# Kernel optimization log

Measured on AMD Instinct MI355X. Metric: run time of the kernel, lower is better.

## Reference

```python
import jax, jax.numpy as jnp
import numpy as np

B, N, DIM = 4, 16384, 3
HID = 128            # hidden_dim
CDIM = 128           # feature_dim
RESO = 128           # plane_resolution
R2 = RESO * RESO
NBLK = 5             # n_blocks


def setup_inputs() -> dict:
    key = jax.random.key(0)
    ks = jax.random.split(key, 8)
    s = 0.02
    return {
        "points": jax.random.uniform(ks[0], (B, N, DIM), jnp.float32),  # normalized to [0,1)
        "fc_pos_w": jax.random.normal(ks[1], (2 * HID, DIM), jnp.float32) * s,
        "fc_pos_b": jnp.zeros((2 * HID,), jnp.float32),
        "blk_fc0_w": jax.random.normal(ks[2], (NBLK, HID, 2 * HID), jnp.float32) * s,
        "blk_fc0_b": jnp.zeros((NBLK, HID), jnp.float32),
        "blk_fc1_w": jax.random.normal(ks[3], (NBLK, HID, HID), jnp.float32) * s,
        "blk_fc1_b": jnp.zeros((NBLK, HID), jnp.float32),
        "blk_sc_w": jax.random.normal(ks[4], (NBLK, HID, 2 * HID), jnp.float32) * s,
        "fc_c_w": jax.random.normal(ks[5], (CDIM, HID), jnp.float32) * s,
        "fc_c_b": jnp.zeros((CDIM,), jnp.float32),
    }


def _coord2index(coord_xy):
    # coordinate2index: (coord * reso).long(), then x + reso * y
    g = jnp.clip((coord_xy * RESO).astype(jnp.int32), 0, RESO - 1)  # (B, N, 2)
    return g[..., 0] + RESO * g[..., 1]  # (B, N)


def _resblock(x, w0, b0, w1, b1, ws):
    # ResnetBlockFC: shortcut(x) + fc_1(relu(fc_0(relu(x))))
    h = jax.nn.relu(x) @ w0.T + b0          # (B, N, HID)
    dx = jax.nn.relu(h) @ w1.T + b1         # (B, N, HID)
    return x @ ws.T + dx


def _forward(points, fc_pos_w, fc_pos_b, blk_fc0_w, blk_fc0_b,
             blk_fc1_w, blk_fc1_b, blk_sc_w, fc_c_w, fc_c_b):
    idx = _coord2index(points[..., :2])          # (B, N) int32 plane-bin ids
    net = points @ fc_pos_w.T + fc_pos_b          # (B, N, 2*HID)
    net = _resblock(net, blk_fc0_w[0], blk_fc0_b[0], blk_fc1_w[0], blk_fc1_b[0], blk_sc_w[0])

    seg_max = jax.vmap(lambda f, i: jax.ops.segment_max(f, i, num_segments=R2))
    for k in range(1, NBLK):
        bins = seg_max(net, idx)                                  # (B, R2, HID); empty bins -inf, never gathered
        pooled = jnp.take_along_axis(bins, idx[:, :, None], axis=1)  # (B, N, HID)
        net = _resblock(jnp.concatenate([net, pooled], axis=2),
                        blk_fc0_w[k], blk_fc0_b[k], blk_fc1_w[k], blk_fc1_b[k], blk_sc_w[k])

    net = jax.nn.relu(net) @ fc_c_w.T + fc_c_b    # (B, N, CDIM)

    # generate_plane_features: scatter_mean into zero-initialized plane
    seg_sum = jax.vmap(lambda f, i: jax.ops.segment_sum(f, i, num_segments=R2))
    sums = seg_sum(net, idx)                                      # (B, R2, CDIM)
    cnt = seg_sum(jnp.ones(idx.shape + (1,), net.dtype), idx)     # (B, R2, 1)
    mean = sums / jnp.maximum(cnt, 1.0)                           # empty bins stay 0
    return jnp.transpose(mean, (0, 2, 1)).reshape(B, CDIM, RESO, RESO)


def reference(points, fc_pos_w, fc_pos_b, blk_fc0_w, blk_fc0_b,
              blk_fc1_w, blk_fc1_b, blk_sc_w, fc_c_w, fc_c_b):
    return _forward(points, fc_pos_w, fc_pos_b, blk_fc0_w, blk_fc0_b,
                    blk_fc1_w, blk_fc1_b, blk_sc_w, fc_c_w, fc_c_b)
```

## Files before the change

### kernel.cpp

```cpp
#include <hip/hip_runtime.h>

#define NBATCH 4
#define NPTS   16384
#define BN     (NBATCH * NPTS)

typedef __attribute__((ext_vector_type(8))) _Float16 half8;
typedef __attribute__((ext_vector_type(4))) float f32x4;

#define INV4096 2.44140625e-4f

__device__ __forceinline__ void splith(float x, _Float16& h, _Float16& l) {
  float ax = __builtin_fabsf(x);
  if (ax < 6.1035e-5f) {
    unsigned short sb = (unsigned short)((__float_as_uint(x) >> 16) & 0x8000u);
    h = __builtin_bit_cast(_Float16, sb);
    l = (_Float16)(x * 4096.f);
  } else {
    _Float16 hh = (_Float16)x;
    h = hh;
    l = (_Float16)((x - (float)hh) * 4096.f);
  }
}
__device__ __forceinline__ void splith8(const float v[8], half8& hi, half8& lo) {
  #pragma unroll
  for (int j = 0; j < 8; ++j) { _Float16 h, l; splith(v[j], h, l); hi[j] = h; lo[j] = l; }
}

__device__ __forceinline__ half8 relu8(half8 sgn, half8 v) {
  uint4 s = __builtin_bit_cast(uint4, sgn);
  uint4 x = __builtin_bit_cast(uint4, v);
  unsigned* sp = (unsigned*)&s;
  unsigned* xp = (unsigned*)&x;
  uint4 out;
  unsigned* op = (unsigned*)&out;
  #pragma unroll
  for (int w = 0; w < 4; ++w) {
    unsigned m = sp[w] & 0x80008000u;
    unsigned drop = (m - (m >> 15)) | m;
    op[w] = xp[w] & ~drop;
  }
  return __builtin_bit_cast(half8, out);
}

__global__ void k_zero4(float4* __restrict__ p, int n4) {
  int g = blockIdx.x * 256 + threadIdx.x;
  if (g < n4) p[g] = make_float4(0.f, 0.f, 0.f, 0.f);
}

__device__ __forceinline__ int bin_of(const float* __restrict__ pts, int g) {
  float px = pts[g * 3 + 0], py = pts[g * 3 + 1];
  int xi = (int)(px * 128.f); xi = xi < 0 ? 0 : (xi > 127 ? 127 : xi);
  int yi = (int)(py * 128.f); yi = yi < 0 ? 0 : (yi > 127 ? 127 : yi);
  return xi + (yi << 7);
}

__global__ void k_idx(const float* __restrict__ pts, int* __restrict__ cnti) {
  int g = blockIdx.x * 256 + threadIdx.x;
  if (g >= BN) return;
  int b = g >> 14;
  atomicAdd(&cnti[(b << 14) + bin_of(pts, g)], 1);
}

__global__ void k_scan(const int* __restrict__ cnti, int* __restrict__ off,
                       int* __restrict__ cursor) {
  __shared__ int part[256];
  const int b = blockIdx.x, t = threadIdx.x;
  const int base = b << 14;
  int s = 0;
  #pragma unroll 8
  for (int i = 0; i < 64; ++i) s += cnti[base + t * 64 + i];
  part[t] = s;
  __syncthreads();
  for (int o = 1; o < 256; o <<= 1) {
    int v = (t >= o) ? part[t - o] : 0;
    __syncthreads();
    part[t] += v;
    __syncthreads();
  }
  int run = base + (t == 0 ? 0 : part[t - 1]);
  #pragma unroll 8
  for (int i = 0; i < 64; ++i) {
    int g = base + t * 64 + i;
    off[g] = run;
    cursor[g] = run;
    run += cnti[g];
  }
}

__global__ void k_scatter(const float* __restrict__ pts, int* __restrict__ cursor,
                          int* __restrict__ perm, int* __restrict__ sbin) {
  int p = blockIdx.x * 256 + threadIdx.x;
  if (p >= BN) return;
  int b = p >> 14;
  int id = bin_of(pts, p);
  int pos = atomicAdd(&cursor[(b << 14) + id], 1);
  perm[pos] = p;
  sbin[pos] = id;
}

__device__ __forceinline__ void pack_slot(const float* __restrict__ src, int K,
                                          _Float16* __restrict__ dhi, int NK,
                                          int slot) {
  int fpt = (K >> 5) << 6;
  int t = slot / fpt, rem = slot - t * fpt;
  int s = rem >> 6, lane = rem & 63;
  int row = (t << 4) + (lane & 15);
  int k0 = (s << 5) + ((lane >> 4) << 3);
  float v[8];
  #pragma unroll
  for (int j = 0; j < 8; ++j) v[j] = src[row * K + k0 + j];
  half8 hi, lo; splith8(v, hi, lo);
  *(half8*)&dhi[(size_t)slot << 3] = hi;
  *(half8*)&dhi[((size_t)slot << 3) + NK] = lo;
}

__global__ void k_pack(const float* __restrict__ fc0w, const float* __restrict__ scw,
                       const float* __restrict__ fc1w, const float* __restrict__ fccw,
                       _Float16* __restrict__ wp) {
  int g = blockIdx.x * 256 + threadIdx.x;
  if (g < 20480) {
    int l = g >> 12, slot = g & 4095;
    pack_slot(fc0w + (size_t)l * 32768, 256, wp + (size_t)l * 65536, 32768, slot);
  } else if (g < 40960) {
    int g2 = g - 20480; int l = g2 >> 12, slot = g2 & 4095;
    pack_slot(scw + (size_t)l * 32768, 256, wp + 327680 + (size_t)l * 65536, 32768, slot);
  } else if (g < 51200) {
    int g2 = g - 40960; int l = g2 >> 11, slot = g2 & 2047;
    pack_slot(fc1w + (size_t)l * 16384, 128, wp + 655360 + (size_t)l * 32768, 16384, slot);
  } else {
    int slot = g - 51200;
    pack_slot(fccw, 128, wp + 819200, 16384, slot);
  }
}

template <int SRC, int MODE>
__launch_bounds__(256, 4)
__global__ void k_rb(const float* __restrict__ pts, const float* __restrict__ netIn,
                     const int* __restrict__ perm, const int* __restrict__ sbin,
                     const int* __restrict__ off_, const int* __restrict__ cnti_,
                     const float* __restrict__ posw, const float* __restrict__ posb,
                     const _Float16* __restrict__ w0p, const float* __restrict__ b0,
                     const _Float16* __restrict__ w1p, const float* __restrict__ b1,
                     const _Float16* __restrict__ wsp,
                     float* __restrict__ netOut,
                     const _Float16* __restrict__ fccp, const float* __restrict__ fccb,
                     float* __restrict__ sums) {
  extern __shared__ _Float16 smem[];
  _Float16* Ahi = smem;
  _Float16* Alo = smem + 8192;
  const int tid = threadIdx.x;
  const int lane = tid & 63, wave = tid >> 6;
  const int p0 = blockIdx.x << 5;
  const int b = p0 >> 14;

  #pragma unroll
  for (int i = 0; i < 4; ++i) {
    int sidx = tid + (i << 8);
    int m = sidx >> 5, kslot = sidx & 31, k0 = kslot << 3;
    float v[8];
    if (SRC == 0) {
      const float* pp = &pts[(size_t)perm[p0 + m] * 3];
      float px = pp[0], py = pp[1], pz = pp[2];
      #pragma unroll
      for (int j = 0; j < 8; ++j) {
        int c = k0 + j;
        v[j] = fmaf(posw[c * 3 + 0], px,
               fmaf(posw[c * 3 + 1], py,
               fmaf(posw[c * 3 + 2], pz, posb[c])));
      }
    } else {
      if (kslot < 16) {
        float4 a = *(const float4*)&netIn[(size_t)(p0 + m) * 128 + k0];
        float4 c = *(const float4*)&netIn[(size_t)(p0 + m) * 128 + k0 + 4];
        v[0] = a.x; v[1] = a.y; v[2] = a.z; v[3] = a.w;
        v[4] = c.x; v[5] = c.y; v[6] = c.z; v[7] = c.w;
      } else {
        int g = (b << 14) + sbin[p0 + m];
        int s0 = off_[g], n = cnti_[g];
        const float* base = &netIn[(size_t)s0 * 128 + (k0 - 128)];
        float4 a = *(const float4*)base;
        float4 c = *(const float4*)(base + 4);
        for (int r = 1; r < n; ++r) {
          const float* rp = base + (size_t)r * 128;
          float4 va = *(const float4*)rp;
          float4 vc = *(const float4*)(rp + 4);
          a.x = fmaxf(a.x, va.x); a.y = fmaxf(a.y, va.y);
          a.z = fmaxf(a.z, va.z); a.w = fmaxf(a.w, va.w);
          c.x = fmaxf(c.x, vc.x); c.y = fmaxf(c.y, vc.y);
          c.z = fmaxf(c.z, vc.z); c.w = fmaxf(c.w, vc.w);
        }
        v[0] = a.x; v[1] = a.y; v[2] = a.z; v[3] = a.w;
        v[4] = c.x; v[5] = c.y; v[6] = c.z; v[7] = c.w;
      }
    }
    half8 hi, lo; splith8(v, hi, lo);
    int mt = m >> 4, mm = m & 15, s = kslot >> 2, quad = kslot & 3;
    int ln = mm + (quad << 4), kg = (mt << 3) + s;
    int u = (kg << 6) + (ln ^ (kg & 7));
    *(half8*)&Ahi[u << 3] = hi;
    *(half8*)&Alo[u << 3] = lo;
  }
  __syncthreads();

  f32x4 hm[2][2], hc[2][2], so[2][2], sc[2][2];
  {
    int col = lane & 15;
    #pragma unroll
    for (int nt = 0; nt < 2; ++nt) {
      float bv0 = b0[(wave << 5) + (nt << 4) + col];
      float bv1 = b1[(wave << 5) + (nt << 4) + col];
      #pragma unroll
      for (int mt = 0; mt < 2; ++mt) {
        hm[mt][nt] = (f32x4){bv0, bv0, bv0, bv0};
        so[mt][nt] = (f32x4){bv1, bv1, bv1, bv1};
        hc[mt][nt] = (f32x4){0.f, 0.f, 0.f, 0.f};
        sc[mt][nt] = (f32x4){0.f, 0.f, 0.f, 0.f};
      }
    }
  }
  const _Float16* w0lo = w0p + 32768;
  const _Float16* wslo = wsp + 32768;

  half8 c0h[2], c0l[2], csh[2], csl[2];
  #pragma unroll
  for (int nt = 0; nt < 2; ++nt) {
    int tw = (wave << 1) + nt;
    size_t fo = (((size_t)(tw << 3) << 6) + lane) << 3;
    c0h[nt] = *(const half8*)&w0p[fo];
    c0l[nt] = *(const half8*)&w0lo[fo];
    csh[nt] = *(const half8*)&wsp[fo];
    csl[nt] = *(const half8*)&wslo[fo];
  }
  #pragma unroll
  for (int ks = 0; ks < 8; ++ks) {
    half8 n0h[2], n0l[2], nsh[2], nsl[2];
    if (ks < 7) {
      #pragma unroll
      for (int nt = 0; nt < 2; ++nt) {
        int tw = (wave << 1) + nt;
        size_t fo = (((size_t)((tw << 3) + ks + 1) << 6) + lane) << 3;
        n0h[nt] = *(const half8*)&w0p[fo];
        n0l[nt] = *(const half8*)&w0lo[fo];
        nsh[nt] = *(const half8*)&wsp[fo];
        nsl[nt] = *(const half8*)&wslo[fo];
      }
    }
    #pragma unroll
    for (int mt = 0; mt < 2; ++mt) {
      int kg = (mt << 3) + ks;
      int u = (kg << 6) + (lane ^ (kg & 7));
      half8 ah = *(const half8*)&Ahi[u << 3];
      half8 al = *(const half8*)&Alo[u << 3];
      half8 arh = relu8(ah, ah);
      half8 arl = relu8(ah, al);
      #pragma unroll
      for (int nt = 0; nt < 2; ++nt) {
        hm[mt][nt] = __builtin_amdgcn_mfma_f32_16x16x32_f16(arh, c0h[nt], hm[mt][nt], 0, 0, 0);
        hc[mt][nt] = __builtin_amdgcn_mfma_f32_16x16x32_f16(arl, c0h[nt], hc[mt][nt], 0, 0, 0);
        hc[mt][nt] = __builtin_amdgcn_mfma_f32_16x16x32_f16(arh, c0l[nt], hc[mt][nt], 0, 0, 0);
        so[mt][nt] = __builtin_amdgcn_mfma_f32_16x16x32_f16(ah,  csh[nt], so[mt][nt], 0, 0, 0);
        sc[mt][nt] = __builtin_amdgcn_mfma_f32_16x16x32_f16(al,  csh[nt], sc[mt][nt], 0, 0, 0);
        sc[mt][nt] = __builtin_amdgcn_mfma_f32_16x16x32_f16(ah,  csl[nt], sc[mt][nt], 0, 0, 0);
      }
    }
    if (ks < 7) {
      #pragma unroll
      for (int nt = 0; nt < 2; ++nt) {
        c0h[nt] = n0h[nt]; c0l[nt] = n0l[nt];
        csh[nt] = nsh[nt]; csl[nt] = nsl[nt];
      }
    }
  }
  __syncthreads();

  _Float16* A2hi = smem;
  _Float16* A2lo = smem + 4096;
  {
    int q = lane >> 4, j2 = lane & 7, qh = (lane & 15) >> 3;
    #pragma unroll
    for (int mt = 0; mt < 2; ++mt) {
      int kg2 = (mt << 2) + wave;
      #pragma unroll
      for (int nt = 0; nt < 2; ++nt) {
        int quad2 = (nt << 1) + qh;
        #pragma unroll
        for (int r = 0; r < 4; ++r) {
          float hv = fmaxf(fmaf(hc[mt][nt][r], INV4096, hm[mt][nt][r]), 0.f);
          _Float16 hb, lb; splith(hv, hb, lb);
          int mm2 = (q << 2) + r;
          int ln2 = mm2 + (quad2 << 4);
          int u2 = (kg2 << 6) + (ln2 ^ (kg2 & 7));
          A2hi[(u2 << 3) + j2] = hb;
          A2lo[(u2 << 3) + j2] = lb;
        }
      }
    }
  }
  __syncthreads();

  const _Float16* w1lo = w1p + 16384;
  half8 w1ch[2], w1cl[2];
  #pragma unroll
  for (int nt = 0; nt < 2; ++nt) {
    int tw = (wave << 1) + nt;
    size_t fo = (((size_t)(tw << 2) << 6) + lane) << 3;
    w1ch[nt] = *(const half8*)&w1p[fo];
    w1cl[nt] = *(const half8*)&w1lo[fo];
  }
  #pragma unroll
  for (int ks = 0; ks < 4; ++ks) {
    half8 nh[2], nl[2];
    if (ks < 3) {
      #pragma unroll
      for (int nt = 0; nt < 2; ++nt) {
        int tw = (wave << 1) + nt;
        size_t fo = (((size_t)((tw << 2) + ks + 1) << 6) + lane) << 3;
        nh[nt] = *(const half8*)&w1p[fo];
        nl[nt] = *(const half8*)&w1lo[fo];
      }
    }
    #pragma unroll
    for (int mt = 0; mt < 2; ++mt) {
      int kg = (mt << 2) + ks;
      int u = (kg << 6) + (lane ^ (kg & 7));
      half8 ah = *(const half8*)&A2hi[u << 3];
      half8 al = *(const half8*)&A2lo[u << 3];
      #pragma unroll
      for (int nt = 0; nt < 2; ++nt) {
        so[mt][nt] = __builtin_amdgcn_mfma_f32_16x16x32_f16(ah, w1ch[nt], so[mt][nt], 0, 0, 0);
        sc[mt][nt] = __builtin_amdgcn_mfma_f32_16x16x32_f16(al, w1ch[nt], sc[mt][nt], 0, 0, 0);
        sc[mt][nt] = __builtin_amdgcn_mfma_f32_16x16x32_f16(ah, w1cl[nt], sc[mt][nt], 0, 0, 0);
      }
    }
    if (ks < 3) {
      #pragma unroll
      for (int nt = 0; nt < 2; ++nt) { w1ch[nt] = nh[nt]; w1cl[nt] = nl[nt]; }
    }
  }

  if (MODE == 0) {
    int col = lane & 15, q = lane >> 4;
    #pragma unroll
    for (int mt = 0; mt < 2; ++mt) {
      #pragma unroll
      for (int r = 0; r < 4; ++r) {
        int m_g = p0 + (mt << 4) + (q << 2) + r;
        #pragma unroll
        for (int nt = 0; nt < 2; ++nt) {
          int n = (wave << 5) + (nt << 4) + col;
          netOut[(size_t)m_g * 128 + n] = fmaf(sc[mt][nt][r], INV4096, so[mt][nt][r]);
        }
      }
    }
  } else {
    float* S = (float*)smem;
    int* Bid = (int*)((char*)smem + 16896);
    __syncthreads();
    {
      int q = lane >> 4, j2 = lane & 7, qh = (lane & 15) >> 3;
      #pragma unroll
      for (int mt = 0; mt < 2; ++mt) {
        int kg2 = (mt << 2) + wave;
        #pragma unroll
        for (int nt = 0; nt < 2; ++nt) {
          int quad2 = (nt << 1) + qh;
          #pragma unroll
          for (int r = 0; r < 4; ++r) {
            float sv = fmaxf(fmaf(sc[mt][nt][r], INV4096, so[mt][nt][r]), 0.f);
            _Float16 hb, lb; splith(sv, hb, lb);
            int mm2 = (q << 2) + r;
            int ln2 = mm2 + (quad2 << 4);
            int u2 = (kg2 << 6) + (ln2 ^ (kg2 & 7));
            A2hi[(u2 << 3) + j2] = hb;
            A2lo[(u2 << 3) + j2] = lb;
          }
        }
      }
    }
    __syncthreads();
    const _Float16* flo = fccp + 16384;
    f32x4 am[2][2], ac[2][2];
    {
      int col = lane & 15;
      #pragma unroll
      for (int nt = 0; nt < 2; ++nt) {
        float bv = fccb[(wave << 5) + (nt << 4) + col];
        #pragma unroll
        for (int mt = 0; mt < 2; ++mt) {
          am[mt][nt] = (f32x4){bv, bv, bv, bv};
          ac[mt][nt] = (f32x4){0.f, 0.f, 0.f, 0.f};
        }
      }
    }
    #pragma unroll
    for (int ks = 0; ks < 4; ++ks) {
      half8 ch[2], cl[2];
      #pragma unroll
      for (int nt = 0; nt < 2; ++nt) {
        int tw = (wave << 1) + nt;
        size_t fo = (((size_t)((tw << 2) + ks) << 6) + lane) << 3;
        ch[nt] = *(const half8*)&fccp[fo];
        cl[nt] = *(const half8*)&flo[fo];
      }
      #pragma unroll
      for (int mt = 0; mt < 2; ++mt) {
        int kg = (mt << 2) + ks;
        int u = (kg << 6) + (lane ^ (kg & 7));
        half8 ah = *(const half8*)&A2hi[u << 3];
        half8 al = *(const half8*)&A2lo[u << 3];
        #pragma unroll
        for (int nt = 0; nt < 2; ++nt) {
          am[mt][nt] = __builtin_amdgcn_mfma_f32_16x16x32_f16(ah, ch[nt], am[mt][nt], 0, 0, 0);
          ac[mt][nt] = __builtin_amdgcn_mfma_f32_16x16x32_f16(al, ch[nt], ac[mt][nt], 0, 0, 0);
          ac[mt][nt] = __builtin_amdgcn_mfma_f32_16x16x32_f16(ah, cl[nt], ac[mt][nt], 0, 0, 0);
        }
      }
    }
    __syncthreads();
    {
      int col = lane & 15, q = lane >> 4;
      #pragma unroll
      for (int mt = 0; mt < 2; ++mt) {
        #pragma unroll
        for (int r = 0; r < 4; ++r) {
          int mrow = (mt << 4) + (q << 2) + r;
          #pragma unroll
          for (int nt = 0; nt < 2; ++nt) {
            int n = (wave << 5) + (nt << 4) + col;
            S[mrow * 132 + n] = fmaf(ac[mt][nt][r], INV4096, am[mt][nt][r]);
          }
        }
      }
      if (tid < 32) Bid[tid] = sbin[p0 + tid];
    }
    __syncthreads();
    {
      int c = tid & 127, h = (tid >> 7) << 4;
      int cur = Bid[h];
      float acc = S[h * 132 + c];
      #pragma unroll
      for (int m2 = 1; m2 < 16; ++m2) {
        int m = h + m2;
        int id = Bid[m];
        float e = S[m * 132 + c];
        if (id != cur) {
          atomicAdd(&sums[(size_t)(((b << 14) + cur) << 7) + c], acc);
          cur = id; acc = e;
        } else acc += e;
      }
      atomicAdd(&sums[(size_t)(((b << 14) + cur) << 7) + c], acc);
    }
  }
}

__launch_bounds__(256)
__global__ void k_finalize(const float* __restrict__ sums, const int* __restrict__ cnti,
                           float* __restrict__ out) {
  __shared__ float t[64 * 65];
  __shared__ float rc[64];
  const int bid = blockIdx.x;
  const int ct = bid & 1, rt = (bid >> 1) & 255, b = bid >> 9;
  const int r0 = rt << 6, c0 = ct << 6;
  const int tid = threadIdx.x, l16 = tid & 15, sl = tid >> 4;
  for (int rr = sl; rr < 64; rr += 16) {
    float4 v = *(const float4*)&sums[(size_t)((b << 14) + r0 + rr) * 128 + c0 + (l16 << 2)];
    int cb = l16 << 2;
    t[rr * 65 + cb + 0] = v.x; t[rr * 65 + cb + 1] = v.y;
    t[rr * 65 + cb + 2] = v.z; t[rr * 65 + cb + 3] = v.w;
  }
  if (tid < 64) rc[tid] = 1.f / fmaxf((float)cnti[(b << 14) + r0 + tid], 1.f);
  __syncthreads();
  for (int cc = sl; cc < 64; cc += 16) {
    int c = c0 + cc;
    int rb = l16 << 2;
    float4 o = make_float4(t[(rb + 0) * 65 + cc] * rc[rb + 0],
                           t[(rb + 1) * 65 + cc] * rc[rb + 1],
                           t[(rb + 2) * 65 + cc] * rc[rb + 2],
                           t[(rb + 3) * 65 + cc] * rc[rb + 3]);
    *(float4*)&out[(size_t)((b << 7) + c) * 16384 + r0 + rb] = o;
  }
}

extern "C" void kernel_launch(void* const* d_in, const int* in_sizes, int n_in,
                              void* d_out, int out_size, void* d_ws, size_t ws_size,
                              hipStream_t stream) {
  const float* points = (const float*)d_in[0];
  const float* posw   = (const float*)d_in[1];
  const float* posb   = (const float*)d_in[2];
  const float* fc0w   = (const float*)d_in[3];
  const float* fc0b   = (const float*)d_in[4];
  const float* fc1w   = (const float*)d_in[5];
  const float* fc1b   = (const float*)d_in[6];
  const float* scw    = (const float*)d_in[7];
  const float* fccw   = (const float*)d_in[8];
  const float* fccb   = (const float*)d_in[9];
  float* outp = (float*)d_out;

  float* net_a = (float*)d_ws;
  float* net_b = net_a + (size_t)BN * 128;
  int* perm   = (int*)(net_b + (size_t)BN * 128);
  int* sbin   = perm + BN;
  int* cnti   = sbin + BN;
  int* off    = cnti + BN;
  int* cursor = off + BN;
  _Float16* wp = (_Float16*)(cursor + BN);

  const _Float16* w0_ = wp;
  const _Float16* ws_ = wp + 327680;
  const _Float16* w1_ = wp + 655360;
  const _Float16* fcc_ = wp + 819200;

  k_zero4<<<64, 256, 0, stream>>>((float4*)cnti, 16384);
  k_idx<<<256, 256, 0, stream>>>(points, cnti);
  k_scan<<<4, 256, 0, stream>>>(cnti, off, cursor);
  k_scatter<<<256, 256, 0, stream>>>(points, cursor, perm, sbin);
  k_pack<<<208, 256, 0, stream>>>(fc0w, scw, fc1w, fccw, wp);

  k_rb<0, 0><<<2048, 256, 32768, stream>>>(points, nullptr, perm, sbin, off, cnti,
                                           posw, posb,
                                           w0_, fc0b, w1_, fc1b, ws_, net_a,
                                           fcc_, fccb, nullptr);
  const float* src = net_a;
  float* dst = net_b;
  for (int l = 1; l < 4; ++l) {
    k_rb<1, 0><<<2048, 256, 32768, stream>>>(points, src, perm, sbin, off, cnti,
                                             posw, posb,
                                             w0_ + (size_t)l * 65536, fc0b + l * 128,
                                             w1_ + (size_t)l * 32768, fc1b + l * 128,
                                             ws_ + (size_t)l * 65536, dst,
                                             fcc_, fccb, nullptr);
    float* t = (float*)src; src = dst; dst = t;
  }
  float* sums = dst;
  k_zero4<<<8192, 256, 0, stream>>>((float4*)sums, 2097152);
  k_rb<1, 1><<<2048, 256, 32768, stream>>>(points, src, perm, sbin, off, cnti,
                                           posw, posb,
                                           w0_ + (size_t)4 * 65536, fc0b + 4 * 128,
                                           w1_ + (size_t)4 * 32768, fc1b + 4 * 128,
                                           ws_ + (size_t)4 * 65536, nullptr,
                                           fcc_, fccb, sums);
  k_finalize<<<2048, 256, 0, stream>>>(sums, cnti, outp);
}
```

Measured before the change: 365.6 us.

## Switch block GEMMs from 16x16x32 to 32x32x16 MFMA tiles

Replaces the 2x2 grid of 16x16x32 MFMA tiles per wave with a single 32x32x16 MFMA tile. This touches the weight packing layout, the LDS A-fragment swizzle, the accumulator indexing and every epilogue. The aim is to cut the instruction count and the number of LDS fragment loads per FLOP. It also unrolls the segment-max gather loop by two so more loads are in flight. The risk is that the larger accumulators raise register pressure, and the new swizzle (flane^kg) may cause different LDS bank conflicts.

Measured after the change: 374.1 us. 1.02x slower.

```diff
diff --git a/kernel.cpp b/kernel.cpp
--- a/kernel.cpp
+++ b/kernel.cpp
@@ -5,7 +5,7 @@
 #define BN     (NBATCH * NPTS)
 
 typedef __attribute__((ext_vector_type(8))) _Float16 half8;
-typedef __attribute__((ext_vector_type(4))) float f32x4;
+typedef __attribute__((ext_vector_type(16))) float f32x16;
 
 #define INV4096 2.44140625e-4f
 
@@ -101,11 +101,11 @@
 __device__ __forceinline__ void pack_slot(const float* __restrict__ src, int K,
                                           _Float16* __restrict__ dhi, int NK,
                                           int slot) {
-  int fpt = (K >> 5) << 6;
+  int fpt = (K >> 4) << 6;
   int t = slot / fpt, rem = slot - t * fpt;
   int s = rem >> 6, lane = rem & 63;
-  int row = (t << 4) + (lane & 15);
-  int k0 = (s << 5) + ((lane >> 4) << 3);
+  int row = (t << 5) + (lane & 31);
+  int k0 = (s << 4) + ((lane >> 5) << 3);
   float v[8];
   #pragma unroll
   for (int j = 0; j < 8; ++j) v[j] = src[row * K + k0 + j];
@@ -180,7 +180,20 @@
         const float* base = &netIn[(size_t)s0 * 128 + (k0 - 128)];
         float4 a = *(const float4*)base;
         float4 c = *(const float4*)(base + 4);
-        for (int r = 1; r < n; ++r) {
+        int r = 1;
+        for (; r + 1 < n; r += 2) {
+          const float* r1 = base + (size_t)r * 128;
+          const float* r2 = r1 + 128;
+          float4 va = *(const float4*)r1;
+          float4 vc = *(const float4*)(r1 + 4);
+          float4 wa = *(const float4*)r2;
+          float4 wc = *(const float4*)(r2 + 4);
+          a.x = fmaxf(a.x, fmaxf(va.x, wa.x)); a.y = fmaxf(a.y, fmaxf(va.y, wa.y));
+          a.z = fmaxf(a.z, fmaxf(va.z, wa.z)); a.w = fmaxf(a.w, fmaxf(va.w, wa.w));
+          c.x = fmaxf(c.x, fmaxf(vc.x, wc.x)); c.y = fmaxf(c.y, fmaxf(vc.y, wc.y));
+          c.z = fmaxf(c.z, fmaxf(vc.z, wc.z)); c.w = fmaxf(c.w, fmaxf(vc.w, wc.w));
+        }
+        if (r < n) {
           const float* rp = base + (size_t)r * 128;
           float4 va = *(const float4*)rp;
           float4 vc = *(const float4*)(rp + 4);
@@ -194,242 +207,157 @@
       }
     }
     half8 hi, lo; splith8(v, hi, lo);
-    int mt = m >> 4, mm = m & 15, s = kslot >> 2, quad = kslot & 3;
-    int ln = mm + (quad << 4), kg = (mt << 3) + s;
-    int u = (kg << 6) + (ln ^ (kg & 7));
+    int kg = kslot >> 1;
+    int flane = ((kslot & 1) << 5) + m;
+    int u = (kg << 6) + (flane ^ kg);
     *(half8*)&Ahi[u << 3] = hi;
     *(half8*)&Alo[u << 3] = lo;
   }
   __syncthreads();
 
-  f32x4 hm[2][2], hc[2][2], so[2][2], sc[2][2];
+  f32x16 hm, hc, so, sc;
   {
-    int col = lane & 15;
+    float bv0 = b0[(wave << 5) + (lane & 31)];
+    float bv1 = b1[(wave << 5) + (lane & 31)];
     #pragma unroll
-    for (int nt = 0; nt < 2; ++nt) {
-      float bv0 = b0[(wave << 5) + (nt << 4) + col];
-      float bv1 = b1[(wave << 5) + (nt << 4) + col];
-      #pragma unroll
-      for (int mt = 0; mt < 2; ++mt) {
-        hm[mt][nt] = (f32x4){bv0, bv0, bv0, bv0};
-        so[mt][nt] = (f32x4){bv1, bv1, bv1, bv1};
-        hc[mt][nt] = (f32x4){0.f, 0.f, 0.f, 0.f};
-        sc[mt][nt] = (f32x4){0.f, 0.f, 0.f, 0.f};
-      }
-    }
+    for (int r = 0; r < 16; ++r) { hm[r] = bv0; so[r] = bv1; hc[r] = 0.f; sc[r] = 0.f; }
   }
   const _Float16* w0lo = w0p + 32768;
   const _Float16* wslo = wsp + 32768;
 
-  half8 c0h[2], c0l[2], csh[2], csl[2];
-  #pragma unroll
-  for (int nt = 0; nt < 2; ++nt) {
-    int tw = (wave << 1) + nt;
-    size_t fo = (((size_t)(tw << 3) << 6) + lane) << 3;
-    c0h[nt] = *(const half8*)&w0p[fo];
-    c0l[nt] = *(const half8*)&w0lo[fo];
-    csh[nt] = *(const half8*)&wsp[fo];
-    csl[nt] = *(const half8*)&wslo[fo];
-  }
-  #pragma unroll
-  for (int ks = 0; ks < 8; ++ks) {
-    half8 n0h[2], n0l[2], nsh[2], nsl[2];
-    if (ks < 7) {
-      #pragma unroll
-      for (int nt = 0; nt < 2; ++nt) {
-        int tw = (wave << 1) + nt;
-        size_t fo = (((size_t)((tw << 3) + ks + 1) << 6) + lane) << 3;
-        n0h[nt] = *(const half8*)&w0p[fo];
-        n0l[nt] = *(const half8*)&w0lo[fo];
-        nsh[nt] = *(const half8*)&wsp[fo];
-        nsl[nt] = *(const half8*)&wslo[fo];
-      }
-    }
-    #pragma unroll
-    for (int mt = 0; mt < 2; ++mt) {
-      int kg = (mt << 3) + ks;
-      int u = (kg << 6) + (lane ^ (kg & 7));
-      half8 ah = *(const half8*)&Ahi[u << 3];
-      half8 al = *(const half8*)&Alo[u << 3];
-      half8 arh = relu8(ah, ah);
-      half8 arl = relu8(ah, al);
-      #pragma unroll
-      for (int nt = 0; nt < 2; ++nt) {
-        hm[mt][nt] = __builtin_amdgcn_mfma_f32_16x16x32_f16(arh, c0h[nt], hm[mt][nt], 0, 0, 0);
-        hc[mt][nt] = __builtin_amdgcn_mfma_f32_16x16x32_f16(arl, c0h[nt], hc[mt][nt], 0, 0, 0);
-        hc[mt][nt] = __builtin_amdgcn_mfma_f32_16x16x32_f16(arh, c0l[nt], hc[mt][nt], 0, 0, 0);
-        so[mt][nt] = __builtin_amdgcn_mfma_f32_16x16x32_f16(ah,  csh[nt], so[mt][nt], 0, 0, 0);
-        sc[mt][nt] = __builtin_amdgcn_mfma_f32_16x16x32_f16(al,  csh[nt], sc[mt][nt], 0, 0, 0);
-        sc[mt][nt] = __builtin_amdgcn_mfma_f32_16x16x32_f16(ah,  csl[nt], sc[mt][nt], 0, 0, 0);
-      }
-    }
-    if (ks < 7) {
-      #pragma unroll
-      for (int nt = 0; nt < 2; ++nt) {
-        c0h[nt] = n0h[nt]; c0l[nt] = n0l[nt];
-        csh[nt] = nsh[nt]; csl[nt] = nsl[nt];
-      }
-    }
+  half8 c0h, c0l, csh, csl;
+  {
+    size_t fo = (((size_t)(wave << 4) << 6) + lane) << 3;
+    c0h = *(const half8*)&w0p[fo];
+    c0l = *(const half8*)&w0lo[fo];
+    csh = *(const half8*)&wsp[fo];
+    csl = *(const half8*)&wslo[fo];
+  }
+  #pragma unroll
+  for (int ks = 0; ks < 16; ++ks) {
+    half8 n0h, n0l, nsh, nsl;
+    if (ks < 15) {
+      size_t fo = (((size_t)((wave << 4) + ks + 1) << 6) + lane) << 3;
+      n0h = *(const half8*)&w0p[fo];
+      n0l = *(const half8*)&w0lo[fo];
+      nsh = *(const half8*)&wsp[fo];
+      nsl = *(const half8*)&wslo[fo];
+    }
+    int u = (ks << 6) + (lane ^ ks);
+    half8 ah = *(const half8*)&Ahi[u << 3];
+    half8 al = *(const half8*)&Alo[u << 3];
+    half8 arh = relu8(ah, ah);
+    half8 arl = relu8(ah, al);
+    hm = __builtin_amdgcn_mfma_f32_32x32x16_f16(arh, c0h, hm, 0, 0, 0);
+    hc = __builtin_amdgcn_mfma_f32_32x32x16_f16(arl, c0h, hc, 0, 0, 0);
+    hc = __builtin_amdgcn_mfma_f32_32x32x16_f16(arh, c0l, hc, 0, 0, 0);
+    so = __builtin_amdgcn_mfma_f32_32x32x16_f16(ah,  csh, so, 0, 0, 0);
+    sc = __builtin_amdgcn_mfma_f32_32x32x16_f16(al,  csh, sc, 0, 0, 0);
+    sc = __builtin_amdgcn_mfma_f32_32x32x16_f16(ah,  csl, sc, 0, 0, 0);
+    if (ks < 15) { c0h = n0h; c0l = n0l; csh = nsh; csl = nsl; }
   }
   __syncthreads();
 
   _Float16* A2hi = smem;
   _Float16* A2lo = smem + 4096;
   {
-    int q = lane >> 4, j2 = lane & 7, qh = (lane & 15) >> 3;
+    int col = lane & 31, hi5 = lane >> 5;
     #pragma unroll
-    for (int mt = 0; mt < 2; ++mt) {
-      int kg2 = (mt << 2) + wave;
-      #pragma unroll
-      for (int nt = 0; nt < 2; ++nt) {
-        int quad2 = (nt << 1) + qh;
-        #pragma unroll
-        for (int r = 0; r < 4; ++r) {
-          float hv = fmaxf(fmaf(hc[mt][nt][r], INV4096, hm[mt][nt][r]), 0.f);
-          _Float16 hb, lb; splith(hv, hb, lb);
-          int mm2 = (q << 2) + r;
-          int ln2 = mm2 + (quad2 << 4);
-          int u2 = (kg2 << 6) + (ln2 ^ (kg2 & 7));
-          A2hi[(u2 << 3) + j2] = hb;
-          A2lo[(u2 << 3) + j2] = lb;
-        }
-      }
+    for (int r = 0; r < 16; ++r) {
+      int m = (r & 3) + ((r >> 2) << 3) + (hi5 << 2);
+      float hv = fmaxf(fmaf(hc[r], INV4096, hm[r]), 0.f);
+      _Float16 hb, lb; splith(hv, hb, lb);
+      int n = (wave << 5) + col;
+      int kg2 = n >> 4;
+      int fl2 = (((n >> 3) & 1) << 5) + m;
+      int u2 = (kg2 << 6) + (fl2 ^ kg2);
+      int j2 = n & 7;
+      A2hi[(u2 << 3) + j2] = hb;
+      A2lo[(u2 << 3) + j2] = lb;
     }
   }
   __syncthreads();
 
   const _Float16* w1lo = w1p + 16384;
-  half8 w1ch[2], w1cl[2];
-  #pragma unroll
-  for (int nt = 0; nt < 2; ++nt) {
-    int tw = (wave << 1) + nt;
-    size_t fo = (((size_t)(tw << 2) << 6) + lane) << 3;
-    w1ch[nt] = *(const half8*)&w1p[fo];
-    w1cl[nt] = *(const half8*)&w1lo[fo];
-  }
-  #pragma unroll
-  for (int ks = 0; ks < 4; ++ks) {
-    half8 nh[2], nl[2];
-    if (ks < 3) {
-      #pragma unroll
-      for (int nt = 0; nt < 2; ++nt) {
-        int tw = (wave << 1) + nt;
-        size_t fo = (((size_t)((tw << 2) + ks + 1) << 6) + lane) << 3;
-        nh[nt] = *(const half8*)&w1p[fo];
-        nl[nt] = *(const half8*)&w1lo[fo];
-      }
-    }
+  half8 w1ch, w1cl;
+  {
+    size_t fo = (((size_t)(wave << 3) << 6) + lane) << 3;
+    w1ch = *(const half8*)&w1p[fo];
+    w1cl = *(const half8*)&w1lo[fo];
+  }
+  #pragma unroll
+  for (int ks = 0; ks < 8; ++ks) {
+    half8 nh, nl;
+    if (ks < 7) {
+      size_t fo = (((size_t)((wave << 3) + ks + 1) << 6) + lane) << 3;
+      nh = *(const half8*)&w1p[fo];
+      nl = *(const half8*)&w1lo[fo];
+    }
+    int u = (ks << 6) + (lane ^ ks);
+    half8 ah = *(const half8*)&A2hi[u << 3];
+    half8 al = *(const half8*)&A2lo[u << 3];
+    so = __builtin_amdgcn_mfma_f32_32x32x16_f16(ah, w1ch, so, 0, 0, 0);
+    sc = __builtin_amdgcn_mfma_f32_32x32x16_f16(al, w1ch, sc, 0, 0, 0);
+    sc = __builtin_amdgcn_mfma_f32_32x32x16_f16(ah, w1cl, sc, 0, 0, 0);
+    if (ks < 7) { w1ch = nh; w1cl = nl; }
+  }
+
+  if (MODE == 0) {
+    int col = lane & 31, hi5 = lane >> 5;
+    int n = (wave << 5) + col;
     #pragma unroll
-    for (int mt = 0; mt < 2; ++mt) {
-      int kg = (mt << 2) + ks;
-      int u = (kg << 6) + (lane ^ (kg & 7));
-      half8 ah = *(const half8*)&A2hi[u << 3];
-      half8 al = *(const half8*)&A2lo[u << 3];
-      #pragma unroll
-      for (int nt = 0; nt < 2; ++nt) {
-        so[mt][nt] = __builtin_amdgcn_mfma_f32_16x16x32_f16(ah, w1ch[nt], so[mt][nt], 0, 0, 0);
-        sc[mt][nt] = __builtin_amdgcn_mfma_f32_16x16x32_f16(al, w1ch[nt], sc[mt][nt], 0, 0, 0);
-        sc[mt][nt] = __builtin_amdgcn_mfma_f32_16x16x32_f16(ah, w1cl[nt], sc[mt][nt], 0, 0, 0);
-      }
-    }
-    if (ks < 3) {
-      #pragma unroll
-      for (int nt = 0; nt < 2; ++nt) { w1ch[nt] = nh[nt]; w1cl[nt] = nl[nt]; }
-    }
-  }
-
-  if (MODE == 0) {
-    int col = lane & 15, q = lane >> 4;
-    #pragma unroll
-    for (int mt = 0; mt < 2; ++mt) {
-      #pragma unroll
-      for (int r = 0; r < 4; ++r) {
-        int m_g = p0 + (mt << 4) + (q << 2) + r;
-        #pragma unroll
-        for (int nt = 0; nt < 2; ++nt) {
-          int n = (wave << 5) + (nt << 4) + col;
-          netOut[(size_t)m_g * 128 + n] = fmaf(sc[mt][nt][r], INV4096, so[mt][nt][r]);
-        }
-      }
+    for (int r = 0; r < 16; ++r) {
+      int m_g = p0 + (r & 3) + ((r >> 2) << 3) + (hi5 << 2);
+      netOut[(size_t)m_g * 128 + n] = fmaf(sc[r], INV4096, so[r]);
     }
   } else {
     float* S = (float*)smem;
     int* Bid = (int*)((char*)smem + 16896);
     __syncthreads();
     {
-      int q = lane >> 4, j2 = lane & 7, qh = (lane & 15) >> 3;
+      int col = lane & 31, hi5 = lane >> 5;
       #pragma unroll
-      for (int mt = 0; mt < 2; ++mt) {
-        int kg2 = (mt << 2) + wave;
-        #pragma unroll
-        for (int nt = 0; nt < 2; ++nt) {
-          int quad2 = (nt << 1) + qh;
-          #pragma unroll
-          for (int r = 0; r < 4; ++r) {
-            float sv = fmaxf(fmaf(sc[mt][nt][r], INV4096, so[mt][nt][r]), 0.f);
-            _Float16 hb, lb; splith(sv, hb, lb);
-            int mm2 = (q << 2) + r;
-            int ln2 = mm2 + (quad2 << 4);
-            int u2 = (kg2 << 6) + (ln2 ^ (kg2 & 7));
-            A2hi[(u2 << 3) + j2] = hb;
-            A2lo[(u2 << 3) + j2] = lb;
-          }
-        }
+      for (int r = 0; r < 16; ++r) {
+        int m = (r & 3) + ((r >> 2) << 3) + (hi5 << 2);
+        float sv = fmaxf(fmaf(sc[r], INV4096, so[r]), 0.f);
+        _Float16 hb, lb; splith(sv, hb, lb);
+        int n = (wave << 5) + col;
+        int kg2 = n >> 4;
+        int fl2 = (((n >> 3) & 1) << 5) + m;
+        int u2 = (kg2 << 6) + (fl2 ^ kg2);
+        int j2 = n & 7;
+        A2hi[(u2 << 3) + j2] = hb;
+        A2lo[(u2 << 3) + j2] = lb;
       }
     }
     __syncthreads();
     const _Float16* flo = fccp + 16384;
-    f32x4 am[2][2], ac[2][2];
+    f32x16 am, ac;
     {
-      int col = lane & 15;
+      float bv = fccb[(wave << 5) + (lane & 31)];
       #pragma unroll
-      for (int nt = 0; nt < 2; ++nt) {
-        float bv = fccb[(wave << 5) + (nt << 4) + col];
-        #pragma unroll
-        for (int mt = 0; mt < 2; ++mt) {
-          am[mt][nt] = (f32x4){bv, bv, bv, bv};
-          ac[mt][nt] = (f32x4){0.f, 0.f, 0.f, 0.f};
-        }
-      }
+      for (int r = 0; r < 16; ++r) { am[r] = bv; ac[r] = 0.f; }
     }
     #pragma unroll
-    for (int ks = 0; ks < 4; ++ks) {
-      half8 ch[2], cl[2];
+    for (int ks = 0; ks < 8; ++ks) {
+      size_t fo = (((size_t)((wave << 3) + ks) << 6) + lane) << 3;
+      half8 ch = *(const half8*)&fccp[fo];
+      half8 cl = *(const half8*)&flo[fo];
+      int u = (ks << 6) + (lane ^ ks);
+      half8 ah = *(const half8*)&A2hi[u << 3];
+      half8 al = *(const half8*)&A2lo[u << 3];
+      am = __builtin_amdgcn_mfma_f32_32x32x16_f16(ah, ch, am, 0, 0, 0);
+      ac = __builtin_amdgcn_mfma_f32_32x32x16_f16(al, ch, ac, 0, 0, 0);
+      ac = __builtin_amdgcn_mfma_f32_32x32x16_f16(ah, cl, ac, 0, 0, 0);
+    }
+    __syncthreads();
+    {
+      int col = lane & 31, hi5 = lane >> 5;
+      int n = (wave << 5) + col;
       #pragma unroll
-      for (int nt = 0; nt < 2; ++nt) {
-        int tw = (wave << 1) + nt;
-        size_t fo = (((size_t)((tw << 2) + ks) << 6) + lane) << 3;
-        ch[nt] = *(const half8*)&fccp[fo];
-        cl[nt] = *(const half8*)&flo[fo];
-      }
-      #pragma unroll
-      for (int mt = 0; mt < 2; ++mt) {
-        int kg = (mt << 2) + ks;
-        int u = (kg << 6) + (lane ^ (kg & 7));
-        half8 ah = *(const half8*)&A2hi[u << 3];
-        half8 al = *(const half8*)&A2lo[u << 3];
-        #pragma unroll
-        for (int nt = 0; nt < 2; ++nt) {
-          am[mt][nt] = __builtin_amdgcn_mfma_f32_16x16x32_f16(ah, ch[nt], am[mt][nt], 0, 0, 0);
-          ac[mt][nt] = __builtin_amdgcn_mfma_f32_16x16x32_f16(al, ch[nt], ac[mt][nt], 0, 0, 0);
-          ac[mt][nt] = __builtin_amdgcn_mfma_f32_16x16x32_f16(ah, cl[nt], ac[mt][nt], 0, 0, 0);
-        }
-      }
-    }
-    __syncthreads();
-    {
-      int col = lane & 15, q = lane >> 4;
-      #pragma unroll
-      for (int mt = 0; mt < 2; ++mt) {
-        #pragma unroll
-        for (int r = 0; r < 4; ++r) {
-          int mrow = (mt << 4) + (q << 2) + r;
-          #pragma unroll
-          for (int nt = 0; nt < 2; ++nt) {
-            int n = (wave << 5) + (nt << 4) + col;
-            S[mrow * 132 + n] = fmaf(ac[mt][nt][r], INV4096, am[mt][nt][r]);
-          }
-        }
+      for (int r = 0; r < 16; ++r) {
+        int mrow = (r & 3) + ((r >> 2) << 3) + (hi5 << 2);
+        S[mrow * 132 + n] = fmaf(ac[r], INV4096, am[r]);
       }
       if (tid < 32) Bid[tid] = sbin[p0 + tid];
     }
```
